# Kernel tuning notes

Measured on AMD Instinct MI355X. Metric: run time of the kernel, lower is better.

Reference implementation:

```python
import jax, jax.numpy as jnp
import numpy as np

B, C, H, W, K = 16, 1, 768, 768, 512


def setup_inputs() -> dict:
    key = jax.random.key(0)
    k1, k2, k3 = jax.random.split(key, 3)
    pre_denses = jax.random.normal(k1, (B, C, H, W), dtype=jnp.float32)
    gt_denses = jax.random.normal(k2, (B, C, H, W), dtype=jnp.float32)
    gt_cors = jax.random.randint(k3, (B, K, 2), 0, min(H, W), dtype=jnp.int32)
    return {"pre_denses": pre_denses, "gt_denses": gt_denses, "gt_cors": gt_cors}


def _peak_mask(pre):
    # The original pads by 2, shift-compares, then crops by 1; this is equivalent
    # to a zero-pad-by-1 4-neighbor local-max test at every original pixel.
    p = jnp.pad(pre, ((0, 0), (0, 0), (1, 1), (1, 1)))
    left = p[:, :, 1:-1, 2:]
    right = p[:, :, 1:-1, :-2]
    up = p[:, :, 2:, 1:-1]
    down = p[:, :, :-2, 1:-1]
    return (pre > left) & (pre > right) & (pre > up) & (pre > down)


def reference(pre_denses, gt_denses, gt_cors):
    b, c, h, w = pre_denses.shape
    # --- loss1: peak-position loss ---
    pre_mask = _peak_mask(pre_denses)  # [B,1,H,W] bool
    batch_idx = jnp.arange(b)[:, None]           # [B,1]
    ys = gt_cors[:, :, 1]                        # row index
    xs = gt_cors[:, :, 0]                        # col index
    gt_mask = jnp.zeros((b, c, h, w), dtype=bool).at[batch_idx, 0, ys, xs].set(True)
    mask1 = jnp.bitwise_xor(pre_mask, gt_mask).astype(jnp.float32)  # C_head = 1
    error = (pre_denses - gt_denses) ** 2
    l1 = jnp.mean(jnp.sum(mask1 * error, axis=(1, 2, 3)))
    # --- loss2: weighted MSE ---
    head = (gt_denses > 0).astype(jnp.float32)
    mse_mask = 5.0 * head + (1.0 - head)  # C_head=5, C_no_head=1
    l2 = jnp.mean(jnp.sum(mse_mask * error, axis=(1, 2, 3)))
    return l1 + l2
```

## Files before the change

### kernel.cpp

```cpp
#include <hip/hip_runtime.h>

#define BDIM 16
#define HDIM 768
#define WDIM 768
#define KCOR 512
#define STRIP 16
constexpr int HW = HDIM * WDIM;
constexpr int QW = WDIM / 4;
constexpr int STRIPS = HDIM / STRIP;
constexpr int NSTRIPB = BDIM * STRIPS;
constexpr int NCORRB = BDIM;
constexpr int NBLK = NSTRIPB + NCORRB;

__global__ __launch_bounds__(QW) void fused_kernel(
    const float* __restrict__ pre,
    const float* __restrict__ gt,
    const int* __restrict__ cors,
    float* __restrict__ out) {

    __shared__ int   table[1024];
    __shared__ float red[3];

    float acc = 0.0f;

    if (blockIdx.x >= NCORRB) {
        const int sid   = blockIdx.x - NCORRB;
        const int b     = sid / STRIPS;
        const int strip = sid % STRIPS;
        const int r0    = strip * STRIP;
        const int t     = threadIdx.x;

        const float* preb = pre + b * HW;
        const float* gtb  = gt  + b * HW;

        int idx = r0 * WDIM + t * 4;

        float4 u4 = (r0 > 0) ? *(const float4*)(preb + idx - WDIM)
                             : make_float4(0.f, 0.f, 0.f, 0.f);
        float4 c4 = *(const float4*)(preb + idx);

        #pragma unroll 4
        for (int r = 0; r < STRIP; ++r) {
            const int row = r0 + r;
            const float4 d4 = (row < HDIM - 1) ? *(const float4*)(preb + idx + WDIM)
                                               : make_float4(0.f, 0.f, 0.f, 0.f);
            const float4 g4 = *(const float4*)(gtb + idx);
            const float lft = (t > 0)      ? preb[idx - 1] : 0.0f;
            const float rgt = (t < QW - 1) ? preb[idx + 4] : 0.0f;

            const float c[4]  = {c4.x, c4.y, c4.z, c4.w};
            const float g[4]  = {g4.x, g4.y, g4.z, g4.w};
            const float u[4]  = {u4.x, u4.y, u4.z, u4.w};
            const float d[4]  = {d4.x, d4.y, d4.z, d4.w};
            const float lr[6] = {lft, c[0], c[1], c[2], c[3], rgt};

            #pragma unroll
            for (int j = 0; j < 4; ++j) {
                const bool peak = (c[j] > lr[j]) && (c[j] > lr[j + 2]) &&
                                  (c[j] > u[j]) && (c[j] > d[j]);
                float e = c[j] - g[j];
                e *= e;
                const float wt = (g[j] > 0.0f ? 5.0f : 1.0f) + (peak ? 1.0f : 0.0f);
                acc += wt * e;
            }

            u4 = c4;
            c4 = d4;
            idx += WDIM;
        }
    } else {
        const int b = blockIdx.x;

        for (int i = threadIdx.x; i < 1024; i += QW) table[i] = -1;
        __syncthreads();

        for (int k = threadIdx.x; k < KCOR; k += QW) {
            const int x = cors[(b * KCOR + k) * 2 + 0];
            const int y = cors[(b * KCOR + k) * 2 + 1];
            const int packed = y * WDIM + x;

            unsigned h = ((unsigned)packed * 2654435761u) >> 22;
            bool mine = false;
            for (;;) {
                const int old = atomicCAS(&table[h], -1, packed);
                if (old == -1)     { mine = true; break; }
                if (old == packed) { break; }
                h = (h + 1) & 1023;
            }

            if (mine) {
                const int idx = b * HW + packed;
                const float c = pre[idx];
                const float l = (x > 0)        ? pre[idx - 1]    : 0.0f;
                const float r = (x < WDIM - 1) ? pre[idx + 1]    : 0.0f;
                const float u = (y > 0)        ? pre[idx - WDIM] : 0.0f;
                const float d = (y < HDIM - 1) ? pre[idx + WDIM] : 0.0f;
                const bool peak = (c > l) && (c > r) && (c > u) && (c > d);
                float e = c - gt[idx];
                e *= e;
                acc += (peak ? -1.0f : 1.0f) * e;
            }
        }
    }

    #pragma unroll
    for (int off = 32; off > 0; off >>= 1) acc += __shfl_down(acc, off);

    const int wave = threadIdx.x >> 6;
    const int lane = threadIdx.x & 63;
    if (lane == 0) red[wave] = acc;
    __syncthreads();
    if (threadIdx.x == 0) {
        atomicAdd(out, (red[0] + red[1] + red[2]) * (1.0f / (float)BDIM));
    }
}

extern "C" void kernel_launch(void* const* d_in, const int* in_sizes, int n_in,
                              void* d_out, int out_size, void* d_ws, size_t ws_size,
                              hipStream_t stream) {
    const float* pre  = (const float*)d_in[0];
    const float* gt   = (const float*)d_in[1];
    const int*   cors = (const int*)d_in[2];

    float* out = (float*)d_out;

    hipMemsetAsync(out, 0, sizeof(float), stream);

    fused_kernel<<<NBLK, QW, 0, stream>>>(pre, gt, cors, out);
}
```

Measured before the change: 111.1 us.

## Use wave shuffles for horizontal neighbors, halve strips, replace atomics with partials

Left and right neighbor values now come from cross-lane shuffles, with global loads kept only for the wave-edge lanes. This removes two scalar global loads per row. The strip height is halved to launch more blocks, and rows are processed in pairs with a launch-bounds occupancy hint. The memset and per-block atomicAdd are replaced by per-block partials plus a small second kernel that reduces them, which adds a second launch.

```diff
diff --git a/kernel.cpp b/kernel.cpp
--- a/kernel.cpp
+++ b/kernel.cpp
@@ -4,7 +4,7 @@
 #define HDIM 768
 #define WDIM 768
 #define KCOR 512
-#define STRIP 16
+#define STRIP 8
 constexpr int HW = HDIM * WDIM;
 constexpr int QW = WDIM / 4;
 constexpr int STRIPS = HDIM / STRIP;
@@ -12,15 +12,18 @@
 constexpr int NCORRB = BDIM;
 constexpr int NBLK = NSTRIPB + NCORRB;
 
-__global__ __launch_bounds__(QW) void fused_kernel(
+typedef float f4v __attribute__((ext_vector_type(4)));
+
+__global__ __launch_bounds__(QW, 6) void fused_kernel(
     const float* __restrict__ pre,
     const float* __restrict__ gt,
     const int* __restrict__ cors,
-    float* __restrict__ out) {
+    float* __restrict__ partials) {
 
     __shared__ int   table[1024];
     __shared__ float red[3];
 
+    const int lane = threadIdx.x & 63;
     float acc = 0.0f;
 
     if (blockIdx.x >= NCORRB) {
@@ -35,25 +38,19 @@
 
         int idx = r0 * WDIM + t * 4;
 
-        float4 u4 = (r0 > 0) ? *(const float4*)(preb + idx - WDIM)
-                             : make_float4(0.f, 0.f, 0.f, 0.f);
-        float4 c4 = *(const float4*)(preb + idx);
+        f4v u4 = (r0 > 0) ? *(const f4v*)(preb + idx - WDIM)
+                          : (f4v){0.f, 0.f, 0.f, 0.f};
+        f4v c4 = *(const f4v*)(preb + idx);
 
-        #pragma unroll 4
-        for (int r = 0; r < STRIP; ++r) {
-            const int row = r0 + r;
-            const float4 d4 = (row < HDIM - 1) ? *(const float4*)(preb + idx + WDIM)
-                                               : make_float4(0.f, 0.f, 0.f, 0.f);
-            const float4 g4 = *(const float4*)(gtb + idx);
-            const float lft = (t > 0)      ? preb[idx - 1] : 0.0f;
-            const float rgt = (t < QW - 1) ? preb[idx + 4] : 0.0f;
+        auto body = [&](const f4v& u, const f4v& c, const f4v& d, const f4v& g,
+                        int rowidx) {
+            const float lw = __shfl_up(c[3], 1);
+            const float rx = __shfl_down(c[0], 1);
+            float lft = lw, rgt = rx;
+            if (lane == 0)  lft = (t > 0)      ? preb[rowidx - 1] : 0.0f;
+            if (lane == 63) rgt = (t < QW - 1) ? preb[rowidx + 4] : 0.0f;
 
-            const float c[4]  = {c4.x, c4.y, c4.z, c4.w};
-            const float g[4]  = {g4.x, g4.y, g4.z, g4.w};
-            const float u[4]  = {u4.x, u4.y, u4.z, u4.w};
-            const float d[4]  = {d4.x, d4.y, d4.z, d4.w};
             const float lr[6] = {lft, c[0], c[1], c[2], c[3], rgt};
-
             #pragma unroll
             for (int j = 0; j < 4; ++j) {
                 const bool peak = (c[j] > lr[j]) && (c[j] > lr[j + 2]) &&
@@ -63,10 +60,29 @@
                 const float wt = (g[j] > 0.0f ? 5.0f : 1.0f) + (peak ? 1.0f : 0.0f);
                 acc += wt * e;
             }
+        };
 
-            u4 = c4;
-            c4 = d4;
-            idx += WDIM;
+        const int hot_pairs = (strip != STRIPS - 1) ? (STRIP / 2) : (STRIP / 2 - 1);
+        #pragma unroll 4
+        for (int k = 0; k < hot_pairs; ++k) {
+            const f4v p1 = *(const f4v*)(preb + idx + WDIM);
+            const f4v p2 = *(const f4v*)(preb + idx + 2 * WDIM);
+            const f4v g1 = *(const f4v*)(gtb + idx);
+            const f4v g2 = *(const f4v*)(gtb + idx + WDIM);
+
+            body(u4, c4, p1, g1, idx);
+            body(c4, p1, p2, g2, idx + WDIM);
+
+            u4 = p1;
+            c4 = p2;
+            idx += 2 * WDIM;
+        }
+        if (strip == STRIPS - 1) {
+            const f4v p1 = *(const f4v*)(preb + idx + WDIM);
+            const f4v g1 = *(const f4v*)(gtb + idx);
+            const f4v g2 = *(const f4v*)(gtb + idx + WDIM);
+            body(u4, c4, p1, g1, idx);
+            body(c4, p1, (f4v){0.f, 0.f, 0.f, 0.f}, g2, idx + WDIM);
         }
     } else {
         const int b = blockIdx.x;
@@ -107,12 +123,24 @@
     for (int off = 32; off > 0; off >>= 1) acc += __shfl_down(acc, off);
 
     const int wave = threadIdx.x >> 6;
-    const int lane = threadIdx.x & 63;
     if (lane == 0) red[wave] = acc;
     __syncthreads();
     if (threadIdx.x == 0) {
-        atomicAdd(out, (red[0] + red[1] + red[2]) * (1.0f / (float)BDIM));
+        partials[blockIdx.x] = red[0] + red[1] + red[2];
     }
+}
+
+__global__ __launch_bounds__(64) void finish_kernel(
+    const float* __restrict__ partials,
+    float* __restrict__ out) {
+
+    float s = 0.0f;
+    for (int i = threadIdx.x; i < NBLK; i += 64) s += partials[i];
+
+    #pragma unroll
+    for (int off = 32; off > 0; off >>= 1) s += __shfl_down(s, off);
+
+    if (threadIdx.x == 0) out[0] = s * (1.0f / (float)BDIM);
 }
 
 extern "C" void kernel_launch(void* const* d_in, const int* in_sizes, int n_in,
@@ -122,9 +150,9 @@
     const float* gt   = (const float*)d_in[1];
     const int*   cors = (const int*)d_in[2];
 
-    float* out = (float*)d_out;
+    float* out      = (float*)d_out;
+    float* partials = (float*)d_ws;
 
-    hipMemsetAsync(out, 0, sizeof(float), stream);
-
-    fused_kernel<<<NBLK, QW, 0, stream>>>(pre, gt, cors, out);
+    fused_kernel<<<NBLK, QW, 0, stream>>>(pre, gt, cors, partials);
+    finish_kernel<<<1, 64, 0, stream>>>(partials, out);
 }
```

New measurement: 108.8 us. -2.0%, faster.
